# Kernel tuning notes

Hardware: AMD Instinct MI355X
Metric: run time of the kernel (lower is better)

## Reference

```python
import jax, jax.numpy as jnp
import numpy as np

N_BOXES = 2048
N_CLASSES = 20


def _cross(a, b):
    return a[..., 0] * b[..., 1] - a[..., 1] * b[..., 0]


def _corners(box):
    # box: [5] = cx, cy, w, h, angle -> [4,2] corner coords
    cx, cy, w, h, a = box[0], box[1], box[2], box[3], box[4]
    c, s = jnp.cos(a), jnp.sin(a)
    dx = jnp.array([-1.0, 1.0, 1.0, -1.0], box.dtype) * (w * 0.5)
    dy = jnp.array([-1.0, -1.0, 1.0, 1.0], box.dtype) * (h * 0.5)
    return jnp.stack([cx + c * dx - s * dy, cy + s * dx + c * dy], axis=-1)


def _points_in_box(pts, box):
    # pts [K,2]; rotate into box frame, test axis-aligned containment
    cx, cy, w, h, a = box[0], box[1], box[2], box[3], box[4]
    c, s = jnp.cos(a), jnp.sin(a)
    px = pts[:, 0] - cx
    py = pts[:, 1] - cy
    lx = c * px + s * py
    ly = -s * px + c * py
    eps = 1e-5
    return (jnp.abs(lx) <= w * 0.5 + eps) & (jnp.abs(ly) <= h * 0.5 + eps)


def _pair_inter_area(box_a, box_b):
    # Exact convex intersection area of two rotated rectangles.
    ca = _corners(box_a)
    cb = _corners(box_b)
    # all 4x4 edge-pair intersections
    p = ca[:, None, :]
    r = (jnp.roll(ca, -1, 0) - ca)[:, None, :]
    q = cb[None, :, :]
    s_ = (jnp.roll(cb, -1, 0) - cb)[None, :, :]
    denom = _cross(r, s_)
    qp = q - p
    safe = jnp.where(jnp.abs(denom) > 1e-9, denom, 1.0)
    t = _cross(qp, s_) / safe
    u = _cross(qp, r) / safe
    valid_e = (jnp.abs(denom) > 1e-9) & (t >= 0.0) & (t <= 1.0) & (u >= 0.0) & (u <= 1.0)
    ipts = p + t[..., None] * r  # [4,4,2]
    # candidate polygon vertices: corners of A in B, corners of B in A, edge crossings
    pts = jnp.concatenate([ca, cb, ipts.reshape(16, 2)], axis=0)  # [24,2]
    mask = jnp.concatenate([_points_in_box(ca, box_b), _points_in_box(cb, box_a), valid_e.reshape(16)], axis=0)
    k = jnp.sum(mask)
    m = mask.astype(pts.dtype)[:, None]
    center = jnp.sum(pts * m, axis=0) / jnp.maximum(k, 1).astype(pts.dtype)
    d = pts - center
    ang = jnp.where(mask, jnp.arctan2(d[:, 1], d[:, 0]), 1e9)  # invalid -> sorted last
    idx = jnp.argsort(ang)
    ds = d[idx]
    ar = jnp.arange(24)
    nxt = jnp.where(ar + 1 < k, ar + 1, 0)
    cr = _cross(ds, ds[nxt])
    area = 0.5 * jnp.abs(jnp.sum(jnp.where(ar < k, cr, 0.0)))
    return jnp.where(k >= 3, area, 0.0)


def _iou_one_vs_many(box, boxes):
    inter = jax.vmap(lambda b: _pair_inter_area(box, b))(boxes)  # [N]
    area_a = box[2] * box[3]
    area_b = boxes[:, 2] * boxes[:, 3]
    return inter / (area_a + area_b - inter + 1e-9)


def _rotated_nms_mask(boxes, scores, iou_threshold):
    # sequential greedy suppression, highest score first; returns bool keep mask (original order)
    n = boxes.shape[0]
    order = jnp.argsort(-scores)
    bs = boxes[order]
    ar = jnp.arange(n)

    def body(i, keep):
        ious = _iou_one_vs_many(bs[i], bs)
        suppress = (ious > iou_threshold) & (ar > i) & keep[i]
        return keep & ~suppress

    keep_sorted = jax.lax.fori_loop(0, n, body, jnp.ones((n,), bool))
    return jnp.zeros((n,), bool).at[order].set(keep_sorted)


def setup_inputs() -> dict:
    key = jax.random.key(0)
    k1, k2, k3, k4, k5 = jax.random.split(key, 5)
    cxcy = jax.random.uniform(k1, (N_BOXES, 2), jnp.float32) * 1024.0
    wh = jax.random.uniform(k2, (N_BOXES, 2), jnp.float32) * 96.0 + 4.0
    ang = jax.random.uniform(k3, (N_BOXES, 1), jnp.float32) * np.pi
    boxes = jnp.concatenate([cxcy, wh, ang], axis=1)  # [N,5]
    scores = jax.random.uniform(k4, (N_BOXES,), jnp.float32)
    labels = jax.random.randint(k5, (N_BOXES,), 0, N_CLASSES, dtype=jnp.int64 if jax.config.read('jax_enable_x64') else jnp.int32)
    return {"boxes": boxes, "scores": scores, "labels": labels, "iou_threshold": 0.5}


def reference(boxes, scores, labels, iou_threshold):
    # multiclass NMS via coordinate-offset trick (N <= 20000 branch of forward)
    cx, cy, w, h = boxes[:, 0], boxes[:, 1], boxes[:, 2], boxes[:, 3]
    max_radius = jnp.max(jnp.sqrt(w * w + h * h)) * 0.5
    max_coord = jnp.maximum(jnp.max(cx), jnp.max(cy))
    offset_scale = (max_coord + max_radius) * 2.0 + 1.0
    offsets = labels.astype(boxes.dtype) * offset_scale
    boxes_nms = boxes.at[:, 0].add(offsets).at[:, 1].add(offsets)
    keep = _rotated_nms_mask(boxes_nms, scores, iou_threshold)
    # fixed-shape encoding of the kept-index set: score of kept boxes, 0 for suppressed
    return scores * keep.astype(scores.dtype)
```

## Files before the change

### kernel.cpp

```cpp
#include <hip/hip_runtime.h>
#include <cstdint>

typedef unsigned long long u64;
typedef uint32_t u32;

#define NB 2048
#define EDGE_CAP 16384
#define CLIST_CAP 2048


__device__ __forceinline__ bool pt_in(float px, float py, float cx, float cy,
                                      float hw, float hh, float c, float s) {
#pragma clang fp contract(off)
  float ax = px - cx;
  float ay = py - cy;
  float lx = c * ax + s * ay;
  float ly = c * ay - s * ax;
  return (fabsf(lx) <= hw + 1e-5f) && (fabsf(ly) <= hh + 1e-5f);
}

__device__ float pair_inter_area(float acx, float acy, float aw, float ah,
                                 float ac, float as_, float bcx, float bcy,
                                 float bw, float bh, float bc, float bs_) {
#pragma clang fp contract(off)
  const float SX[4] = {-1.f, 1.f, 1.f, -1.f};
  const float SY[4] = {-1.f, -1.f, 1.f, 1.f};
  float axx[4], ayy[4], bxx[4], byy[4];
  float ahw = aw * 0.5f, ahh = ah * 0.5f;
  float bhw = bw * 0.5f, bhh = bh * 0.5f;
#pragma unroll
  for (int q = 0; q < 4; ++q) {
    float dx = SX[q] * ahw, dy = SY[q] * ahh;
    axx[q] = acx + ac * dx - as_ * dy;
    ayy[q] = acy + as_ * dx + ac * dy;
    float ex = SX[q] * bhw, ey = SY[q] * bhh;
    bxx[q] = bcx + bc * ex - bs_ * ey;
    byy[q] = bcy + bs_ * ex + bc * ey;
  }
  float px_[24], py_[24];
  bool mk[24];
#pragma unroll
  for (int q = 0; q < 4; ++q) {
    px_[q] = axx[q]; py_[q] = ayy[q];
    mk[q] = pt_in(axx[q], ayy[q], bcx, bcy, bhw, bhh, bc, bs_);
    px_[4 + q] = bxx[q]; py_[4 + q] = byy[q];
    mk[4 + q] = pt_in(bxx[q], byy[q], acx, acy, ahw, ahh, ac, as_);
  }
#pragma unroll
  for (int e = 0; e < 4; ++e) {
    float rx = axx[(e + 1) & 3] - axx[e];
    float ry = ayy[(e + 1) & 3] - ayy[e];
#pragma unroll
    for (int f = 0; f < 4; ++f) {
      float sx = bxx[(f + 1) & 3] - bxx[f];
      float sy = byy[(f + 1) & 3] - byy[f];
      float denom = rx * sy - ry * sx;
      float qpx = bxx[f] - axx[e];
      float qpy = byy[f] - ayy[e];
      bool dn = fabsf(denom) > 1e-9f;
      float safe = dn ? denom : 1.0f;
      float t = (qpx * sy - qpy * sx) / safe;
      float uu = (qpx * ry - qpy * rx) / safe;
      bool valid = dn && (t >= 0.0f) && (t <= 1.0f) && (uu >= 0.0f) && (uu <= 1.0f);
      int id = 8 + e * 4 + f;
      px_[id] = axx[e] + t * rx;
      py_[id] = ayy[e] + t * ry;
      mk[id] = valid;
    }
  }
  int k = 0;
  float sx0 = 0.0f, sy0 = 0.0f;
#pragma unroll
  for (int q = 0; q < 24; ++q) {
    if (mk[q]) { k++; sx0 += px_[q]; sy0 += py_[q]; }
  }
  float kk = (float)(k > 0 ? k : 1);
  float cxm = sx0 / kk, cym = sy0 / kk;
  u64 key[32];
  float dxr[32], dyr[32];
#pragma unroll
  for (int q = 0; q < 24; ++q) {
    float dx = px_[q] - cxm, dy = py_[q] - cym;
    dxr[q] = dx; dyr[q] = dy;
    float ang = mk[q] ? atan2f(dy, dx) : 1e9f;
    u32 ub = __float_as_uint(ang);
    u32 v = (ub & 0x80000000u) ? ~ub : (ub | 0x80000000u);
    key[q] = (((u64)v) << 5) | (u64)q;
  }
#pragma unroll
  for (int q = 24; q < 32; ++q) { key[q] = ~0ull; dxr[q] = 0.f; dyr[q] = 0.f; }
#pragma unroll
  for (int kk2 = 2; kk2 <= 32; kk2 <<= 1) {
#pragma unroll
    for (int jj = kk2 >> 1; jj > 0; jj >>= 1) {
#pragma unroll
      for (int ii = 0; ii < 32; ++ii) {
        int ll = ii ^ jj;
        if (ll > ii) {
          bool up = ((ii & kk2) == 0);
          u64 ka = key[ii], kb = key[ll];
          bool sw = up ? (ka > kb) : (ka < kb);
          key[ii] = sw ? kb : ka;
          key[ll] = sw ? ka : kb;
          float da = dxr[ii], db = dxr[ll];
          dxr[ii] = sw ? db : da;
          dxr[ll] = sw ? da : db;
          float ea = dyr[ii], eb = dyr[ll];
          dyr[ii] = sw ? eb : ea;
          dyr[ll] = sw ? ea : eb;
        }
      }
    }
  }
  float acc = 0.0f;
#pragma unroll
  for (int q = 0; q < 24; ++q) {
    if (q < k - 1) {
      acc += dxr[q] * dyr[q + 1] - dyr[q] * dxr[q + 1];
    } else if (q == k - 1) {
      acc += dxr[q] * dyr[0] - dyr[q] * dxr[0];
    }
  }
  float area = 0.5f * fabsf(acc);
  return (k >= 3) ? area : 0.0f;
}

__global__ __launch_bounds__(256) void build_kernel(
    const float* __restrict__ boxes, const float* __restrict__ scores,
    const int* __restrict__ labels,
    float* __restrict__ cxp, float* __restrict__ cyp, float* __restrict__ wp,
    float* __restrict__ hp, float* __restrict__ cp, float* __restrict__ sp,
    float* __restrict__ radp, float* __restrict__ sscp, int* __restrict__ sidx,
    u32* __restrict__ counters) {
#pragma clang fp contract(off)
  __shared__ float sc[NB];
  __shared__ float smc[4], smr[4];
  int t = threadIdx.x;
  if (blockIdx.x == 0 && t < 4) counters[t] = 0u;
  float mc = -1e30f, mr = -1e30f;
  for (int k = t; k < NB; k += 256) {
    float cx = boxes[k * 5 + 0];
    float cy = boxes[k * 5 + 1];
    float w = boxes[k * 5 + 2];
    float h = boxes[k * 5 + 3];
    mc = fmaxf(mc, fmaxf(cx, cy));
    float ww = w * w;
    float hh = h * h;
    mr = fmaxf(mr, sqrtf(ww + hh));
    sc[k] = scores[k];
  }
  for (int off = 32; off > 0; off >>= 1) {
    mc = fmaxf(mc, __shfl_down(mc, off));
    mr = fmaxf(mr, __shfl_down(mr, off));
  }
  if ((t & 63) == 0) { smc[t >> 6] = mc; smr[t >> 6] = mr; }
  __syncthreads();
  mc = fmaxf(fmaxf(smc[0], smc[1]), fmaxf(smc[2], smc[3]));
  mr = fmaxf(fmaxf(smr[0], smr[1]), fmaxf(smr[2], smr[3]));
  float osc = (mc + mr * 0.5f) * 2.0f + 1.0f;

  int wave = t >> 6, lane = t & 63;
  int i = blockIdx.x * 4 + wave;
  float si = sc[i];
  int rank = 0;
#pragma unroll 8
  for (int m = 0; m < NB / 64; ++m) {
    int j = m * 64 + lane;
    float sj = sc[j];
    rank += (int)((sj > si) || (sj == si && j < i));
  }
  for (int off = 32; off > 0; off >>= 1) rank += __shfl_down(rank, off);
  if (lane == 0) {
    float off = (float)labels[i] * osc;
    float cx = boxes[i * 5 + 0] + off;
    float cy = boxes[i * 5 + 1] + off;
    float w = boxes[i * 5 + 2];
    float h = boxes[i * 5 + 3];
    float a = boxes[i * 5 + 4];
    float c = cosf(a);
    float s = sinf(a);
    float ww = w * w;
    float hh = h * h;
    cxp[rank] = cx;
    cyp[rank] = cy;
    wp[rank] = w;
    hp[rank] = h;
    cp[rank] = c;
    sp[rank] = s;
    radp[rank] = 0.5f * sqrtf(ww + hh);
    sscp[rank] = si;
    sidx[rank] = i;
  }
}

__global__ __launch_bounds__(256) void candgeom_greedy_kernel(
    const float* __restrict__ cxp, const float* __restrict__ cyp,
    const float* __restrict__ wp, const float* __restrict__ hp,
    const float* __restrict__ cp, const float* __restrict__ sp,
    const float* __restrict__ radp, const float* __restrict__ thrp,
    const float* __restrict__ sscp, const int* __restrict__ sidx,
    u32* __restrict__ edges, u32* __restrict__ counters,
    float* __restrict__ out) {
#pragma clang fp contract(off)
  __shared__ float lx[NB], ly[NB], lr[NB];
  __shared__ u32 clist[CLIST_CAP];
  __shared__ u32 ccnt;
  __shared__ int is_last;
  __shared__ u64 keepw[32];
  __shared__ u32 Sw32[64];
  __shared__ int changed;
  int t = threadIdx.x;
  if (t == 0) ccnt = 0;
  for (int k = t; k < NB; k += 256) {
    lx[k] = cxp[k];
    ly[k] = cyp[k];
    lr[k] = radp[k];
  }
  __syncthreads();
  int i0 = blockIdx.x * 8;
#pragma unroll
  for (int di = 0; di < 8; ++di) {
    int i = i0 + di;
    float ax = lx[i], ay = ly[i], ar = lr[i];
#pragma unroll
    for (int c = 0; c < 8; ++c) {
      int j = c * 256 + t;
      if (j > i) {
        float dx = lx[j] - ax, dy = ly[j] - ay;
        float rr = ar + lr[j] + 1.0f;
        if (dx * dx + dy * dy <= rr * rr) {
          u32 s = atomicAdd(&ccnt, 1u);
          if (s < CLIST_CAP) clist[s] = ((u32)i << 16) | (u32)j;
        }
      }
    }
  }
  __syncthreads();
  u32 cnt = ccnt < CLIST_CAP ? ccnt : CLIST_CAP;
  float thr = *thrp;
  for (u32 idx = t; idx < cnt; idx += 256) {
    u32 pk = clist[idx];
    int i = (int)(pk >> 16);
    int j = (int)(pk & 0xFFFFu);
    float acx = cxp[i], acy = cyp[i], aw = wp[i], ah = hp[i];
    float ac = cp[i], as_ = sp[i];
    float bcx = cxp[j], bcy = cyp[j], bw = wp[j], bh = hp[j];
    float bc = cp[j], bs_ = sp[j];
    float inter = pair_inter_area(acx, acy, aw, ah, ac, as_,
                                  bcx, bcy, bw, bh, bc, bs_);
    float areaA = aw * ah;
    float areaB = bw * bh;
    float iou = inter / (areaA + areaB - inter + 1e-9f);
    if (iou > thr) {
      u32 e = atomicAdd(&counters[1], 1u);
      if (e < EDGE_CAP) edges[e] = pk;
    }
  }
  __syncthreads();
  if (t == 0) {
    __threadfence();
    u32 old = atomicAdd(&counters[2], 1u);
    is_last = (old == (u32)(gridDim.x - 1)) ? 1 : 0;
  }
  __syncthreads();
  if (!is_last) return;
  __threadfence();
  __syncthreads();
  u32 ecnt = counters[1];
  if (ecnt > EDGE_CAP) ecnt = EDGE_CAP;
  u32 nl = ecnt < CLIST_CAP ? ecnt : CLIST_CAP;
  for (u32 k = t; k < nl; k += 256) clist[k] = edges[k];
  if (t < 32) keepw[t] = ~0ull;
  __syncthreads();
  for (int iter = 0; iter < 2060; ++iter) {
    if (t < 64) Sw32[t] = 0u;
    if (t == 0) changed = 0;
    __syncthreads();
    for (u32 k = t; k < ecnt; k += 256) {
      u32 pk = (k < CLIST_CAP) ? clist[k] : edges[k];
      int i = (int)(pk >> 16);
      int j = (int)(pk & 0xFFFFu);
      if ((keepw[i >> 6] >> (i & 63)) & 1ull)
        atomicOr(&Sw32[j >> 5], 1u << (j & 31));
    }
    __syncthreads();
    if (t < 32) {
      u64 S = ((u64)Sw32[2 * t]) | (((u64)Sw32[2 * t + 1]) << 32);
      u64 nk = ~S;
      if (nk != keepw[t]) { keepw[t] = nk; changed = 1; }
    }
    __syncthreads();
    int ch = changed;
    __syncthreads();
    if (!ch) break;
  }
  for (int p = t; p < NB; p += 256) {
    int bit = (int)((keepw[p >> 6] >> (p & 63)) & 1ull);
    out[sidx[p]] = bit ? sscp[p] : 0.0f;
  }
}

extern "C" void kernel_launch(void* const* d_in, const int* in_sizes, int n_in,
                              void* d_out, int out_size, void* d_ws, size_t ws_size,
                              hipStream_t stream) {
  const float* boxes = (const float*)d_in[0];
  const float* scores = (const float*)d_in[1];
  const int* labels = (const int*)d_in[2];
  const float* thr = (const float*)d_in[3];
  float* out = (float*)d_out;

  char* base = (char*)d_ws;
  u32* counters = (u32*)base;
  float* arr = (float*)(base + 256);
  float* cxp = arr + 0 * NB;
  float* cyp = arr + 1 * NB;
  float* wp = arr + 2 * NB;
  float* hp = arr + 3 * NB;
  float* cp = arr + 4 * NB;
  float* sp = arr + 5 * NB;
  float* radp = arr + 6 * NB;
  float* sscp = arr + 7 * NB;
  int* sidx = (int*)(base + 66048);
  u32* edges = (u32*)(base + 81920);

  build_kernel<<<512, 256, 0, stream>>>(boxes, scores, labels, cxp, cyp, wp, hp,
                                        cp, sp, radp, sscp, sidx, counters);
  candgeom_greedy_kernel<<<256, 256, 0, stream>>>(cxp, cyp, wp, hp, cp, sp,
                                                  radp, thr, sscp, sidx,
                                                  edges, counters, out);
}
```

Before: 91.46 us.

## Inline intersection, sort keys only with pseudo-angle, gather points from LDS

```diff
diff --git a/kernel.cpp b/kernel.cpp
--- a/kernel.cpp
+++ b/kernel.cpp
@@ -7,123 +7,6 @@
 #define NB 2048
 #define EDGE_CAP 16384
 #define CLIST_CAP 2048
-
-
-__device__ __forceinline__ bool pt_in(float px, float py, float cx, float cy,
-                                      float hw, float hh, float c, float s) {
-#pragma clang fp contract(off)
-  float ax = px - cx;
-  float ay = py - cy;
-  float lx = c * ax + s * ay;
-  float ly = c * ay - s * ax;
-  return (fabsf(lx) <= hw + 1e-5f) && (fabsf(ly) <= hh + 1e-5f);
-}
-
-__device__ float pair_inter_area(float acx, float acy, float aw, float ah,
-                                 float ac, float as_, float bcx, float bcy,
-                                 float bw, float bh, float bc, float bs_) {
-#pragma clang fp contract(off)
-  const float SX[4] = {-1.f, 1.f, 1.f, -1.f};
-  const float SY[4] = {-1.f, -1.f, 1.f, 1.f};
-  float axx[4], ayy[4], bxx[4], byy[4];
-  float ahw = aw * 0.5f, ahh = ah * 0.5f;
-  float bhw = bw * 0.5f, bhh = bh * 0.5f;
-#pragma unroll
-  for (int q = 0; q < 4; ++q) {
-    float dx = SX[q] * ahw, dy = SY[q] * ahh;
-    axx[q] = acx + ac * dx - as_ * dy;
-    ayy[q] = acy + as_ * dx + ac * dy;
-    float ex = SX[q] * bhw, ey = SY[q] * bhh;
-    bxx[q] = bcx + bc * ex - bs_ * ey;
-    byy[q] = bcy + bs_ * ex + bc * ey;
-  }
-  float px_[24], py_[24];
-  bool mk[24];
-#pragma unroll
-  for (int q = 0; q < 4; ++q) {
-    px_[q] = axx[q]; py_[q] = ayy[q];
-    mk[q] = pt_in(axx[q], ayy[q], bcx, bcy, bhw, bhh, bc, bs_);
-    px_[4 + q] = bxx[q]; py_[4 + q] = byy[q];
-    mk[4 + q] = pt_in(bxx[q], byy[q], acx, acy, ahw, ahh, ac, as_);
-  }
-#pragma unroll
-  for (int e = 0; e < 4; ++e) {
-    float rx = axx[(e + 1) & 3] - axx[e];
-    float ry = ayy[(e + 1) & 3] - ayy[e];
-#pragma unroll
-    for (int f = 0; f < 4; ++f) {
-      float sx = bxx[(f + 1) & 3] - bxx[f];
-      float sy = byy[(f + 1) & 3] - byy[f];
-      float denom = rx * sy - ry * sx;
-      float qpx = bxx[f] - axx[e];
-      float qpy = byy[f] - ayy[e];
-      bool dn = fabsf(denom) > 1e-9f;
-      float safe = dn ? denom : 1.0f;
-      float t = (qpx * sy - qpy * sx) / safe;
-      float uu = (qpx * ry - qpy * rx) / safe;
-      bool valid = dn && (t >= 0.0f) && (t <= 1.0f) && (uu >= 0.0f) && (uu <= 1.0f);
-      int id = 8 + e * 4 + f;
-      px_[id] = axx[e] + t * rx;
-      py_[id] = ayy[e] + t * ry;
-      mk[id] = valid;
-    }
-  }
-  int k = 0;
-  float sx0 = 0.0f, sy0 = 0.0f;
-#pragma unroll
-  for (int q = 0; q < 24; ++q) {
-    if (mk[q]) { k++; sx0 += px_[q]; sy0 += py_[q]; }
-  }
-  float kk = (float)(k > 0 ? k : 1);
-  float cxm = sx0 / kk, cym = sy0 / kk;
-  u64 key[32];
-  float dxr[32], dyr[32];
-#pragma unroll
-  for (int q = 0; q < 24; ++q) {
-    float dx = px_[q] - cxm, dy = py_[q] - cym;
-    dxr[q] = dx; dyr[q] = dy;
-    float ang = mk[q] ? atan2f(dy, dx) : 1e9f;
-    u32 ub = __float_as_uint(ang);
-    u32 v = (ub & 0x80000000u) ? ~ub : (ub | 0x80000000u);
-    key[q] = (((u64)v) << 5) | (u64)q;
-  }
-#pragma unroll
-  for (int q = 24; q < 32; ++q) { key[q] = ~0ull; dxr[q] = 0.f; dyr[q] = 0.f; }
-#pragma unroll
-  for (int kk2 = 2; kk2 <= 32; kk2 <<= 1) {
-#pragma unroll
-    for (int jj = kk2 >> 1; jj > 0; jj >>= 1) {
-#pragma unroll
-      for (int ii = 0; ii < 32; ++ii) {
-        int ll = ii ^ jj;
-        if (ll > ii) {
-          bool up = ((ii & kk2) == 0);
-          u64 ka = key[ii], kb = key[ll];
-          bool sw = up ? (ka > kb) : (ka < kb);
-          key[ii] = sw ? kb : ka;
-          key[ll] = sw ? ka : kb;
-          float da = dxr[ii], db = dxr[ll];
-          dxr[ii] = sw ? db : da;
-          dxr[ll] = sw ? da : db;
-          float ea = dyr[ii], eb = dyr[ll];
-          dyr[ii] = sw ? eb : ea;
-          dyr[ll] = sw ? ea : eb;
-        }
-      }
-    }
-  }
-  float acc = 0.0f;
-#pragma unroll
-  for (int q = 0; q < 24; ++q) {
-    if (q < k - 1) {
-      acc += dxr[q] * dyr[q + 1] - dyr[q] * dxr[q + 1];
-    } else if (q == k - 1) {
-      acc += dxr[q] * dyr[0] - dyr[q] * dxr[0];
-    }
-  }
-  float area = 0.5f * fabsf(acc);
-  return (k >= 3) ? area : 0.0f;
-}
 
 __global__ __launch_bounds__(256) void build_kernel(
     const float* __restrict__ boxes, const float* __restrict__ scores,
@@ -204,6 +87,8 @@
 #pragma clang fp contract(off)
   __shared__ float lx[NB], ly[NB], lr[NB];
   __shared__ u32 clist[CLIST_CAP];
+  __shared__ float dxL[256 * 25];
+  __shared__ float dyL[256 * 25];
   __shared__ u32 ccnt;
   __shared__ int is_last;
   __shared__ u64 keepw[32];
@@ -238,16 +123,130 @@
   __syncthreads();
   u32 cnt = ccnt < CLIST_CAP ? ccnt : CLIST_CAP;
   float thr = *thrp;
+  float* myDx = &dxL[t * 25];
+  float* myDy = &dyL[t * 25];
   for (u32 idx = t; idx < cnt; idx += 256) {
     u32 pk = clist[idx];
-    int i = (int)(pk >> 16);
-    int j = (int)(pk & 0xFFFFu);
-    float acx = cxp[i], acy = cyp[i], aw = wp[i], ah = hp[i];
-    float ac = cp[i], as_ = sp[i];
-    float bcx = cxp[j], bcy = cyp[j], bw = wp[j], bh = hp[j];
-    float bc = cp[j], bs_ = sp[j];
-    float inter = pair_inter_area(acx, acy, aw, ah, ac, as_,
-                                  bcx, bcy, bw, bh, bc, bs_);
+    int bi = (int)(pk >> 16);
+    int bj = (int)(pk & 0xFFFFu);
+    float acx = lx[bi], acy = ly[bi], aw = wp[bi], ah = hp[bi];
+    float ac = cp[bi], as_ = sp[bi];
+    float bcx = lx[bj], bcy = ly[bj], bw = wp[bj], bh = hp[bj];
+    float bc = cp[bj], bs_ = sp[bj];
+    const float SX[4] = {-1.f, 1.f, 1.f, -1.f};
+    const float SY[4] = {-1.f, -1.f, 1.f, 1.f};
+    float axx[4], ayy[4], bxx[4], byy[4];
+    float ahw = aw * 0.5f, ahh = ah * 0.5f;
+    float bhw = bw * 0.5f, bhh = bh * 0.5f;
+#pragma unroll
+    for (int q = 0; q < 4; ++q) {
+      float dx = SX[q] * ahw, dy = SY[q] * ahh;
+      axx[q] = acx + ac * dx - as_ * dy;
+      ayy[q] = acy + as_ * dx + ac * dy;
+      float ex = SX[q] * bhw, ey = SY[q] * bhh;
+      bxx[q] = bcx + bc * ex - bs_ * ey;
+      byy[q] = bcy + bs_ * ex + bc * ey;
+    }
+    float px_[24], py_[24];
+    bool mk[24];
+#pragma unroll
+    for (int q = 0; q < 4; ++q) {
+      {
+        float axp = axx[q] - bcx, ayp = ayy[q] - bcy;
+        float lxx = bc * axp + bs_ * ayp;
+        float lyy = bc * ayp - bs_ * axp;
+        mk[q] = (fabsf(lxx) <= bhw + 1e-5f) && (fabsf(lyy) <= bhh + 1e-5f);
+        px_[q] = axx[q]; py_[q] = ayy[q];
+      }
+      {
+        float axp = bxx[q] - acx, ayp = byy[q] - acy;
+        float lxx = ac * axp + as_ * ayp;
+        float lyy = ac * ayp - as_ * axp;
+        mk[4 + q] = (fabsf(lxx) <= ahw + 1e-5f) && (fabsf(lyy) <= ahh + 1e-5f);
+        px_[4 + q] = bxx[q]; py_[4 + q] = byy[q];
+      }
+    }
+#pragma unroll
+    for (int e = 0; e < 4; ++e) {
+      float rx = axx[(e + 1) & 3] - axx[e];
+      float ry = ayy[(e + 1) & 3] - ayy[e];
+#pragma unroll
+      for (int f = 0; f < 4; ++f) {
+        float sx = bxx[(f + 1) & 3] - bxx[f];
+        float sy = byy[(f + 1) & 3] - byy[f];
+        float denom = rx * sy - ry * sx;
+        float qpx = bxx[f] - axx[e];
+        float qpy = byy[f] - ayy[e];
+        bool dn = fabsf(denom) > 1e-9f;
+        float safe = dn ? denom : 1.0f;
+        float tt = (qpx * sy - qpy * sx) / safe;
+        float uu = (qpx * ry - qpy * rx) / safe;
+        bool valid = dn && (tt >= 0.0f) && (tt <= 1.0f) && (uu >= 0.0f) && (uu <= 1.0f);
+        int id = 8 + e * 4 + f;
+        px_[id] = axx[e] + tt * rx;
+        py_[id] = ayy[e] + tt * ry;
+        mk[id] = valid;
+      }
+    }
+    int k = 0;
+    float sx0 = 0.0f, sy0 = 0.0f;
+#pragma unroll
+    for (int q = 0; q < 24; ++q) {
+      if (mk[q]) { k++; sx0 += px_[q]; sy0 += py_[q]; }
+    }
+    float kkf = (float)(k > 0 ? k : 1);
+    float cxm = sx0 / kkf, cym = sy0 / kkf;
+    u64 key[32];
+#pragma unroll
+    for (int q = 0; q < 24; ++q) {
+      float dx = px_[q] - cxm, dy = py_[q] - cym;
+      myDx[q] = dx; myDy[q] = dy;
+      float sm = fabsf(dx) + fabsf(dy);
+      float r = (sm > 0.0f) ? dy / sm : 0.0f;
+      float pa;
+      if (dx >= 0.0f) pa = r;
+      else pa = (__float_as_uint(dy) >> 31) ? (-2.0f - r) : (2.0f - r);
+      float ang = mk[q] ? pa : 1e9f;
+      u32 ub = __float_as_uint(ang);
+      u32 v = (ub & 0x80000000u) ? ~ub : (ub | 0x80000000u);
+      key[q] = (((u64)v) << 5) | (u64)q;
+    }
+#pragma unroll
+    for (int q = 24; q < 32; ++q) key[q] = ~0ull;
+#pragma unroll
+    for (int kk2 = 2; kk2 <= 32; kk2 <<= 1) {
+#pragma unroll
+      for (int jj = kk2 >> 1; jj > 0; jj >>= 1) {
+#pragma unroll
+        for (int ii = 0; ii < 32; ++ii) {
+          int ll = ii ^ jj;
+          if (ll > ii) {
+            bool up = ((ii & kk2) == 0);
+            u64 ka = key[ii], kb = key[ll];
+            bool sw = up ? (ka > kb) : (ka < kb);
+            key[ii] = sw ? kb : ka;
+            key[ll] = sw ? ka : kb;
+          }
+        }
+      }
+    }
+    float acc = 0.0f;
+    int id0 = (int)(key[0] & 31ull);
+    float fx = myDx[id0], fy = myDy[id0];
+    float curx = fx, cury = fy;
+#pragma unroll
+    for (int q = 0; q < 24; ++q) {
+      if (q < k - 1) {
+        int idn = (int)(key[q + 1] & 31ull);
+        float nx = myDx[idn], ny = myDy[idn];
+        acc += curx * ny - cury * nx;
+        curx = nx; cury = ny;
+      } else if (q == k - 1) {
+        acc += curx * fy - cury * fx;
+      }
+    }
+    float area = 0.5f * fabsf(acc);
+    float inter = (k >= 3) ? area : 0.0f;
     float areaA = aw * ah;
     float areaB = bw * bh;
     float iou = inter / (areaA + areaB - inter + 1e-9f);
```

Measured after the change: 88.78 us. 1.03x faster.
